# Optimization experiments

Hardware: AMD Instinct MI355X
Metric: run time of the kernel (lower is better)

## Reference

```python
import jax, jax.numpy as jnp
import numpy as np

LMAX, MMAX = 4, 2
K = (LMAX + 1) ** 2                                 # 25 SH coefficients (l-major node layout)
NL = [LMAX - m + 1 for m in range(MMAX + 1)]        # coeffs per order m: [5,4,3]
M_COEFF = NL[0] + sum(2 * n for n in NL[1:])        # 19 coeffs in m-major (mmax-truncated) edge layout
SPHERE_C, HIDDEN_C = 64, 64
NUM_HEADS, ALPHA_C, VALUE_C, OUT_C = 8, 32, 16, 64
P_GRID = 100
N_NODES, N_EDGES = 4096, 24576
NUM_SPECIES, EDGE_C, EMB_C = 90, 64, 64
N_EXTRA = NUM_HEADS * ALPHA_C + HIDDEN_C            # extra m=0 channels for S2_SEP: alpha + gate scalars


def _ln(x, g, b, eps=1e-5):
    mu = jnp.mean(x, -1, keepdims=True)
    var = jnp.var(x, -1, keepdims=True)
    return (x - mu) * jax.lax.rsqrt(var + eps) * g + b


def _smooth_leaky_relu(x, neg=0.2):
    return 0.5 * (1.0 + neg) * x + 0.5 * (1.0 - neg) * x * (2.0 * jax.nn.sigmoid(x) - 1.0)


def _segment_softmax(a, seg, n):
    amax = jax.lax.stop_gradient(jax.ops.segment_max(a, seg, num_segments=n))
    amax = jnp.where(jnp.isfinite(amax), amax, 0.0)
    e = jnp.exp(a - amax[seg])
    s = jax.ops.segment_sum(e, seg, num_segments=n)
    return e / (s[seg] + 1e-16)


def _so2_conv(x, w0, b0, wms, c_in, c_out, x_edge=None, n_extra=0):
    # x: [E, M_COEFF, c_in] in m-major layout (m=0 block, then per m: real rows then imag rows)
    E = x.shape[0]
    L0 = NL[0]
    x0 = x[:, :L0, :].reshape(E, L0 * c_in)
    if x_edge is not None:
        x0 = x0 * x_edge[:, :L0 * c_in]
    y0 = x0 @ w0 + b0
    extra = None
    if n_extra:
        extra = y0[:, L0 * c_out:]
        y0 = y0[:, :L0 * c_out]
    outs = [y0.reshape(E, L0, c_out)]
    off, rad = L0, L0 * c_in
    for m in range(1, MMAX + 1):
        nl = NL[m]
        xr = x[:, off:off + nl, :]
        xi = x[:, off + nl:off + 2 * nl, :]
        if x_edge is not None:
            s = x_edge[:, rad:rad + nl * c_in].reshape(E, nl, c_in)
            xr, xi = xr * s, xi * s
        xr = xr.reshape(E, nl * c_in)
        xi = xi.reshape(E, nl * c_in)
        half = nl * c_out
        wa, wb = wms[m - 1][:, :half], wms[m - 1][:, half:]
        yr = (xr @ wa - xi @ wb).reshape(E, nl, c_out)  # complex block-matmul
        yi = (xr @ wb + xi @ wa).reshape(E, nl, c_out)
        outs.append(jnp.concatenate([yr, yi], axis=1))
        off += 2 * nl
        rad += nl * c_in
    return jnp.concatenate(outs, axis=1), extra


def setup_inputs():
    key = jax.random.key(0)
    ks = iter(jax.random.split(key, 48))
    def w(shape, fan_in):
        return jax.random.normal(next(ks), shape, jnp.float32) / np.sqrt(fan_in)
    inp = {}
    inp['node_feats'] = jax.random.normal(next(ks), (N_NODES, K, SPHERE_C), jnp.float32)
    inp['node_species'] = jax.random.randint(next(ks), (N_NODES,), 0, NUM_SPECIES)
    inp['edge_distances'] = jax.random.normal(next(ks), (N_EDGES, EDGE_C), jnp.float32)
    inp['senders'] = jax.random.randint(next(ks), (N_EDGES,), 0, N_NODES)
    inp['receivers'] = jax.random.randint(next(ks), (N_EDGES,), 0, N_NODES)
    inp['wigner'] = jax.random.normal(next(ks), (N_EDGES, M_COEFF, K), jnp.float32) / np.sqrt(K)
    inp['snd_emb'] = jax.random.normal(next(ks), (NUM_SPECIES, EMB_C), jnp.float32) * 0.001
    inp['rcv_emb'] = jax.random.normal(next(ks), (NUM_SPECIES, EMB_C), jnp.float32) * 0.001
    ec = EDGE_C + 2 * EMB_C                              # 192 after atom-edge embedding concat
    n_rad = 2 * SPHERE_C * (NL[0] + NL[1] + NL[2])       # 1536 per-edge scales for conv1
    inp['rad_w1'] = w((ec, 64), ec); inp['rad_b1'] = jnp.zeros((64,))
    inp['rad_g1'] = jnp.ones((64,)); inp['rad_be1'] = jnp.zeros((64,))
    inp['rad_w2'] = w((64, 64), 64); inp['rad_b2'] = jnp.zeros((64,))
    inp['rad_g2'] = jnp.ones((64,)); inp['rad_be2'] = jnp.zeros((64,))
    inp['rad_w3'] = w((64, n_rad), 64); inp['rad_b3'] = jnp.ones((n_rad,))
    cin1 = 2 * SPHERE_C
    inp['c1_w0'] = w((NL[0] * cin1, NL[0] * HIDDEN_C + N_EXTRA), NL[0] * cin1)
    inp['c1_b0'] = jnp.zeros((NL[0] * HIDDEN_C + N_EXTRA,))
    inp['c1_wm1'] = w((NL[1] * cin1, 2 * NL[1] * HIDDEN_C), NL[1] * cin1)
    inp['c1_wm2'] = w((NL[2] * cin1, 2 * NL[2] * HIDDEN_C), NL[2] * cin1)
    inp['aln_g'] = jnp.ones((ALPHA_C,)); inp['aln_b'] = jnp.zeros((ALPHA_C,))
    inp['alpha_dot'] = w((NUM_HEADS, ALPHA_C), ALPHA_C)
    inp['to_grid'] = jax.random.normal(next(ks), (P_GRID, M_COEFF), jnp.float32) / np.sqrt(M_COEFF)
    inp['from_grid'] = jax.random.normal(next(ks), (M_COEFF, P_GRID), jnp.float32) / np.sqrt(P_GRID)
    cv = NUM_HEADS * VALUE_C
    inp['c2_w0'] = w((NL[0] * HIDDEN_C, NL[0] * cv), NL[0] * HIDDEN_C)
    inp['c2_b0'] = jnp.zeros((NL[0] * cv,))
    inp['c2_wm1'] = w((NL[1] * HIDDEN_C, 2 * NL[1] * cv), NL[1] * HIDDEN_C)
    inp['c2_wm2'] = w((NL[2] * HIDDEN_C, 2 * NL[2] * cv), NL[2] * HIDDEN_C)
    inp['proj_w'] = w((LMAX + 1, cv, OUT_C), cv)
    inp['proj_b'] = jnp.zeros((OUT_C,))
    return inp


def reference(node_feats, node_species, edge_distances, senders, receivers, wigner,
              snd_emb, rcv_emb, rad_w1, rad_b1, rad_g1, rad_be1, rad_w2, rad_b2,
              rad_g2, rad_be2, rad_w3, rad_b3, c1_w0, c1_b0, c1_wm1, c1_wm2,
              aln_g, aln_b, alpha_dot, to_grid, from_grid,
              c2_w0, c2_b0, c2_wm1, c2_wm2, proj_w, proj_b):
    N = node_feats.shape[0]
    # atom-edge embedding gathers + concat with radial-basis distances
    edge_embeds = jnp.concatenate([edge_distances,
                                   snd_emb[node_species[senders]],
                                   rcv_emb[node_species[receivers]]], axis=1)
    msgs = jnp.concatenate([node_feats[senders], node_feats[receivers]], axis=2)  # [E,25,128]
    msgs = jnp.einsum('emk,ekc->emc', wigner, msgs)                               # rotate to edge frame [E,19,128]
    # radial function -> per-edge input scales for SO2 conv 1
    h = jax.nn.silu(_ln(edge_embeds @ rad_w1 + rad_b1, rad_g1, rad_be1))
    h = jax.nn.silu(_ln(h @ rad_w2 + rad_b2, rad_g2, rad_be2))
    x_edge = h @ rad_w3 + rad_b3
    msgs, x0_extra = _so2_conv(msgs, c1_w0, c1_b0, [c1_wm1, c1_wm2],
                               2 * SPHERE_C, HIDDEN_C, x_edge, N_EXTRA)
    x0_alpha = x0_extra[:, :NUM_HEADS * ALPHA_C]
    x0_gate = x0_extra[:, NUM_HEADS * ALPHA_C:]
    # separable S2 activation: SiLU on sphere grid for l>0, SiLU on scalars for l=0
    grid = jax.nn.silu(jnp.einsum('pm,emc->epc', to_grid, msgs))
    tens = jnp.einsum('mp,epc->emc', from_grid, grid)
    msgs = jnp.concatenate([jax.nn.silu(x0_gate)[:, None, :], tens[:, 1:, :]], axis=1)
    msgs, _ = _so2_conv(msgs, c2_w0, c2_b0, [c2_wm1, c2_wm2], HIDDEN_C, NUM_HEADS * VALUE_C)
    # attention weights: LN -> SmoothLeakyReLU -> dot -> per-receiver softmax
    a = _smooth_leaky_relu(_ln(x0_alpha.reshape(-1, NUM_HEADS, ALPHA_C), aln_g, aln_b))
    alpha = _segment_softmax(jnp.einsum('ehk,hk->eh', a, alpha_dot), receivers, N)
    attn = msgs.reshape(-1, M_COEFF, NUM_HEADS, VALUE_C) * alpha[:, None, :, None]
    msgs = attn.reshape(-1, M_COEFF, NUM_HEADS * VALUE_C)
    msgs = jnp.einsum('emk,emc->ekc', wigner, msgs)    # rotate back (W^T), [E,25,128]
    node = jax.ops.segment_sum(msgs, receivers, num_segments=N)
    # SO3 linear: per-degree-l channel mixing, bias only on l=0
    l_of_k = jnp.asarray(np.repeat(np.arange(LMAX + 1), 2 * np.arange(LMAX + 1) + 1))
    out = jnp.einsum('nkc,kcd->nkd', node, proj_w[l_of_k])
    return out.at[:, 0, :].add(proj_b)
```

## Files before the change

### kernel.cpp

```cpp
#include <hip/hip_runtime.h>

typedef unsigned short u16;
typedef unsigned int u32;
typedef __attribute__((ext_vector_type(8))) short short8;
typedef __attribute__((ext_vector_type(4))) float floatx4;

#define E_EDGES 24576
#define EC 12288
#define N_NODES_C 4096

__device__ __forceinline__ float bf2f(u16 u) {
    union { u32 i; float f; } v; v.i = ((u32)u) << 16; return v.f;
}
__device__ __forceinline__ u16 f2bf(float f) {
    union { float f; u32 i; } v; v.f = f;
    u32 x = v.i;
    u32 r = (x + 0x7fffu + ((x >> 16) & 1u)) >> 16;
    return (u16)r;
}
__device__ __forceinline__ u32 pk_bf16(float a, float b) {
    u32 r;
    asm("v_cvt_pk_bf16_f32 %0, %1, %2" : "=v"(r) : "v"(a), "v"(b));
    return r;
}
__device__ __forceinline__ u32 encf(float f) {
    union { float f; u32 i; } v; v.f = f;
    return (v.i & 0x80000000u) ? ~v.i : (v.i | 0x80000000u);
}
__device__ __forceinline__ float decf(u32 u) {
    union { u32 i; float f; } v;
    v.i = (u & 0x80000000u) ? (u ^ 0x80000000u) : ~u;
    return v.f;
}
__device__ __forceinline__ float sigmoidf_(float x) { return __fdividef(1.f, 1.f + __expf(-x)); }
__device__ __forceinline__ float siluf_(float x) { return x * __fdividef(1.f, 1.f + __expf(-x)); }

__device__ __forceinline__ void gld16(const u16* g, u16* l) {
    __builtin_amdgcn_global_load_lds((const __attribute__((address_space(1))) unsigned int*)g,
                                     (__attribute__((address_space(3))) unsigned int*)l, 16, 0, 0);
}

__global__ void k_diag(float* __restrict__ out, int n) {
    int i = blockIdx.x * 256 + threadIdx.x;
    if (i < n) out[i] = 1000.0f;
}

struct PrepArgs {
    const float *rad_w1, *rad_w2, *rad_w3, *c1_w0, *c2_w0;
    const float *c1_wm1, *c1_wm2, *c2_wm1, *c2_wm2;
    const float *to_grid, *from_grid, *proj_w;
    u16 *w_rad1T, *w_rad2T, *w_rad3T, *w_c1w0T, *w_c2w0T;
    u16 *w_c1m1T, *w_c1m2T, *w_c2m1T, *w_c2m2T;
    u16 *w_tgP, *w_fgP, *w_pwT;
    u32 *nmax; float *nsum; u32 *c_deg;
    const float *dist; const int *species, *snd, *rcv;
    const float *semb, *remb; u16 *ee;
};

__device__ __forceinline__ void prep_transpose(const float* __restrict__ src, u16* __restrict__ dst,
                                               int K, int N, int idx) {
    if (idx >= K * N) return;
    int k = idx / N, n = idx % N;
    dst[n * K + k] = f2bf(src[idx]);
}
__device__ __forceinline__ void prep_combine(const float* __restrict__ src, u16* __restrict__ dst,
                                             int K, int H, int idx) {
    if (idx >= 4 * K * H) return;
    int n = idx / (2 * K), k = idx % (2 * K);
    float v;
    if (k < K) v = src[k * 2 * H + n];
    else {
        int kk = k - K;
        if (n < H) v = -src[kk * 2 * H + H + n];
        else       v = src[kk * 2 * H + (n - H)];
    }
    dst[idx] = f2bf(v);
}

#define PB0 48
#define PB1 16
#define PB2 384
#define PB3 1600
#define PB4 800
#define PB5 2048
#define PB6 1152
#define PB7 2048
#define PB8 1152
#define PB9 30
#define PB10 160
#define PB11 128
#define PB12 16
#define PB13 18432
#define PREP_BLOCKS (PB0+PB1+PB2+PB3+PB4+PB5+PB6+PB7+PB8+PB9+PB10+PB11+PB12+PB13)

__global__ __launch_bounds__(256) void k_prep(PrepArgs a) {
    int bid = blockIdx.x;
    int tid = threadIdx.x;
    if (bid < PB0) { prep_transpose(a.rad_w1, a.w_rad1T, 192, 64, bid * 256 + tid); return; }
    bid -= PB0;
    if (bid < PB1) { prep_transpose(a.rad_w2, a.w_rad2T, 64, 64, bid * 256 + tid); return; }
    bid -= PB1;
    if (bid < PB2) { prep_transpose(a.rad_w3, a.w_rad3T, 64, 1536, bid * 256 + tid); return; }
    bid -= PB2;
    if (bid < PB3) { prep_transpose(a.c1_w0, a.w_c1w0T, 640, 640, bid * 256 + tid); return; }
    bid -= PB3;
    if (bid < PB4) { prep_transpose(a.c2_w0, a.w_c2w0T, 320, 640, bid * 256 + tid); return; }
    bid -= PB4;
    if (bid < PB5) { prep_combine(a.c1_wm1, a.w_c1m1T, 512, 256, bid * 256 + tid); return; }
    bid -= PB5;
    if (bid < PB6) { prep_combine(a.c1_wm2, a.w_c1m2T, 384, 192, bid * 256 + tid); return; }
    bid -= PB6;
    if (bid < PB7) { prep_combine(a.c2_wm1, a.w_c2m1T, 256, 512, bid * 256 + tid); return; }
    bid -= PB7;
    if (bid < PB8) { prep_combine(a.c2_wm2, a.w_c2m2T, 192, 384, bid * 256 + tid); return; }
    bid -= PB8;
    if (bid < PB9) {
        int idx = bid * 256 + tid;
        if (idx < 112 * 32) {
            int p = idx >> 5, m = idx & 31;
            a.w_tgP[idx] = (p < 100 && m < 19) ? f2bf(a.to_grid[p * 19 + m]) : (u16)0;
        }
        int j = idx - 112 * 32;
        if (j >= 0 && j < 32 * 128) {
            int m = j >> 7, k = j & 127;
            a.w_fgP[j] = (m < 19 && k < 100) ? f2bf(a.from_grid[m * 100 + k]) : (u16)0;
        }
        return;
    }
    bid -= PB9;
    if (bid < PB10) {
        int idx = bid * 256 + tid;
        int l = idx >> 13, rem = idx & 8191;
        prep_transpose(a.proj_w + (size_t)l * 8192, a.w_pwT + (size_t)l * 8192, 128, 64, rem);
        return;
    }
    bid -= PB10;
    if (bid < PB11) {
        int idx = bid * 256 + tid;
        if (idx < N_NODES_C * 8) { a.nmax[idx] = 0x007FFFFFu; a.nsum[idx] = 0.f; }
        return;
    }
    bid -= PB11;
    if (bid < PB12) {
        int idx = bid * 256 + tid;
        if (idx < N_NODES_C) a.c_deg[idx] = 0u;
        return;
    }
    bid -= PB12;
    {
        int idx = bid * 256 + tid;
        if (idx >= E_EDGES * 192) return;
        int e = idx / 192, c = idx % 192;
        float v;
        if (c < 64)       v = a.dist[e * 64 + c];
        else if (c < 128) v = a.semb[a.species[a.snd[e]] * 64 + (c - 64)];
        else              v = a.remb[a.species[a.rcv[e]] * 64 + (c - 128)];
        a.ee[idx] = f2bf(v);
    }
}

__global__ void k_deg(const int* __restrict__ rcv, u32* __restrict__ deg) {
    int e = blockIdx.x * 256 + threadIdx.x;
    if (e < E_EDGES) atomicAdd(&deg[rcv[e]], 1u);
}
__global__ __launch_bounds__(256) void k_pfx(const u32* __restrict__ deg,
                                             u32* __restrict__ rowstart, u32* __restrict__ cur) {
    __shared__ u32 ps[256];
    int t = threadIdx.x;
    u32 loc[16]; u32 s = 0;
#pragma unroll
    for (int i = 0; i < 16; i++) { loc[i] = s; s += deg[t * 16 + i]; }
    ps[t] = s;
    __syncthreads();
    for (int o = 1; o < 256; o <<= 1) {
        u32 v = (t >= o) ? ps[t - o] : 0u;
        __syncthreads();
        ps[t] += v;
        __syncthreads();
    }
    u32 base = (t == 0) ? 0u : ps[t - 1];
#pragma unroll
    for (int i = 0; i < 16; i++) { u32 v = base + loc[i]; rowstart[t * 16 + i] = v; cur[t * 16 + i] = v; }
}
__global__ void k_fill(const int* __restrict__ rcv, u32* __restrict__ cur, int* __restrict__ elist) {
    int e = blockIdx.x * 256 + threadIdx.x;
    if (e < E_EDGES) { u32 p = atomicAdd(&cur[rcv[e]], 1u); elist[p] = e; }
}

__global__ __launch_bounds__(256) void k_gemm(
    const u16* __restrict__ A, int lda,
    const u16* __restrict__ BT, int ldb,
    u16* __restrict__ C, int ldc,
    int N, int K,
    const float* __restrict__ bias) {
    __shared__ u16 As[2][128 * 32];
    __shared__ u16 Bs[2][128 * 32];
    int tid = threadIdx.x;
    int bm0 = blockIdx.x * 128;
    int bn0 = blockIdx.y * 128;
    int wave = tid >> 6, lane = tid & 63;
    int wm = (wave >> 1) * 64, wn = (wave & 1) * 64;
    int lrow = lane & 15, lk = (lane >> 4) * 8;

    int srow = (wave << 4) + (lane >> 2);
    int schunk = (lane & 3) << 3;
    const u16* Arow0 = A + (size_t)(bm0 + srow) * lda + schunk;
    const u16* Arow1 = A + (size_t)(bm0 + srow + 64) * lda + schunk;
    int n0 = bn0 + srow;      if (n0 >= N) n0 = N - 1;
    int n1 = bn0 + srow + 64; if (n1 >= N) n1 = N - 1;
    const u16* Brow0 = BT + (size_t)n0 * ldb + schunk;
    const u16* Brow1 = BT + (size_t)n1 * ldb + schunk;

    auto stage = [&](int buf, int k0) {
        gld16(Arow0 + k0, &As[buf][srow * 32 + schunk]);
        gld16(Arow1 + k0, &As[buf][(srow + 64) * 32 + schunk]);
        gld16(Brow0 + k0, &Bs[buf][srow * 32 + schunk]);
        gld16(Brow1 + k0, &Bs[buf][(srow + 64) * 32 + schunk]);
    };

    floatx4 acc[4][4];
#pragma unroll
    for (int i = 0; i < 4; i++)
#pragma unroll
        for (int j = 0; j < 4; j++) acc[i][j] = floatx4{0.f, 0.f, 0.f, 0.f};

    int NT = K >> 5;
    stage(0, 0);
    for (int kt = 0; kt < NT; kt++) {
        int cur = kt & 1;
        if (kt + 1 < NT) {
            stage(cur ^ 1, (kt + 1) << 5);
            asm volatile("s_waitcnt vmcnt(4)" ::: "memory");
        } else {
            asm volatile("s_waitcnt vmcnt(0)" ::: "memory");
        }
        __syncthreads();
        short8 a[4], b[4];
#pragma unroll
        for (int i = 0; i < 4; i++) a[i] = *(const short8*)(&As[cur][(wm + i * 16 + lrow) * 32 + lk]);
#pragma unroll
        for (int j = 0; j < 4; j++) b[j] = *(const short8*)(&Bs[cur][(wn + j * 16 + lrow) * 32 + lk]);
#pragma unroll
        for (int i = 0; i < 4; i++)
#pragma unroll
            for (int j = 0; j < 4; j++)
                acc[i][j] = __builtin_amdgcn_mfma_f32_16x16x32_bf16(b[j], a[i], acc[i][j], 0, 0, 0);
        __syncthreads();
    }

    int q = lane >> 4;
#pragma unroll
    for (int i = 0; i < 4; i++) {
        int row = bm0 + wm + i * 16 + lrow;
#pragma unroll
        for (int j = 0; j < 4; j++) {
            int col = bn0 + wn + j * 16 + q * 4;
            if (col < N) {
                float4 bv = bias ? *(const float4*)(&bias[col]) : float4{0.f, 0.f, 0.f, 0.f};
                uint2 pv;
                pv.x = pk_bf16(acc[i][j][0] + bv.x, acc[i][j][1] + bv.y);
                pv.y = pk_bf16(acc[i][j][2] + bv.z, acc[i][j][3] + bv.w);
                *(uint2*)(&C[(size_t)row * ldc + col]) = pv;
            }
        }
    }
}

struct GemmDesc {
    const u16* A; const u16* BT; u16* C;
    const float* bias;
    int lda, ldb, ldc, N, K;
};
struct Gemm3 {
    GemmDesc d[3];
    int cut0, cut1;
};
__global__ __launch_bounds__(256) void k_gemm3(Gemm3 g) {
    int y = blockIdx.y;
    GemmDesc d;
    int ytile;
    if (y < g.cut0)      { d = g.d[0]; ytile = y; }
    else if (y < g.cut1) { d = g.d[1]; ytile = y - g.cut0; }
    else                 { d = g.d[2]; ytile = y - g.cut1; }

    __shared__ u16 As[2][128 * 32];
    __shared__ u16 Bs[2][128 * 32];
    int tid = threadIdx.x;
    int bm0 = blockIdx.x * 128;
    int bn0 = ytile * 128;
    int wave = tid >> 6, lane = tid & 63;
    int wm = (wave >> 1) * 64, wn = (wave & 1) * 64;
    int lrow = lane & 15, lk = (lane >> 4) * 8;

    int srow = (wave << 4) + (lane >> 2);
    int schunk = (lane & 3) << 3;
    const u16* Arow0 = d.A + (size_t)(bm0 + srow) * d.lda + schunk;
    const u16* Arow1 = d.A + (size_t)(bm0 + srow + 64) * d.lda + schunk;
    int n0 = bn0 + srow;      if (n0 >= d.N) n0 = d.N - 1;
    int n1 = bn0 + srow + 64; if (n1 >= d.N) n1 = d.N - 1;
    const u16* Brow0 = d.BT + (size_t)n0 * d.ldb + schunk;
    const u16* Brow1 = d.BT + (size_t)n1 * d.ldb + schunk;

    auto stage = [&](int buf, int k0) {
        gld16(Arow0 + k0, &As[buf][srow * 32 + schunk]);
        gld16(Arow1 + k0, &As[buf][(srow + 64) * 32 + schunk]);
        gld16(Brow0 + k0, &Bs[buf][srow * 32 + schunk]);
        gld16(Brow1 + k0, &Bs[buf][(srow + 64) * 32 + schunk]);
    };

    floatx4 acc[4][4];
#pragma unroll
    for (int i = 0; i < 4; i++)
#pragma unroll
        for (int j = 0; j < 4; j++) acc[i][j] = floatx4{0.f, 0.f, 0.f, 0.f};

    int NT = d.K >> 5;
    stage(0, 0);
    for (int kt = 0; kt < NT; kt++) {
        int cur = kt & 1;
        if (kt + 1 < NT) {
            stage(cur ^ 1, (kt + 1) << 5);
            asm volatile("s_waitcnt vmcnt(4)" ::: "memory");
        } else {
            asm volatile("s_waitcnt vmcnt(0)" ::: "memory");
        }
        __syncthreads();
        short8 a[4], b[4];
#pragma unroll
        for (int i = 0; i < 4; i++) a[i] = *(const short8*)(&As[cur][(wm + i * 16 + lrow) * 32 + lk]);
#pragma unroll
        for (int j = 0; j < 4; j++) b[j] = *(const short8*)(&Bs[cur][(wn + j * 16 + lrow) * 32 + lk]);
#pragma unroll
        for (int i = 0; i < 4; i++)
#pragma unroll
            for (int j = 0; j < 4; j++)
                acc[i][j] = __builtin_amdgcn_mfma_f32_16x16x32_bf16(b[j], a[i], acc[i][j], 0, 0, 0);
        __syncthreads();
    }

    int q = lane >> 4;
#pragma unroll
    for (int i = 0; i < 4; i++) {
        int row = bm0 + wm + i * 16 + lrow;
#pragma unroll
        for (int j = 0; j < 4; j++) {
            int col = bn0 + wn + j * 16 + q * 4;
            if (col < d.N) {
                float4 bv = d.bias ? *(const float4*)(&d.bias[col]) : float4{0.f, 0.f, 0.f, 0.f};
                uint2 pv;
                pv.x = pk_bf16(acc[i][j][0] + bv.x, acc[i][j][1] + bv.y);
                pv.y = pk_bf16(acc[i][j][2] + bv.z, acc[i][j][3] + bv.w);
                *(uint2*)(&d.C[(size_t)row * d.ldc + col]) = pv;
            }
        }
    }
}

__global__ __launch_bounds__(256) void k_ln_silu(const u16* __restrict__ in, u16* __restrict__ out,
                                                 const float* __restrict__ g, const float* __restrict__ b) {
    int tid = threadIdx.x;
    int e = blockIdx.x * 4 + (tid >> 6);
    int c = tid & 63;
    float x = bf2f(in[(size_t)e * 64 + c]);
    float s = x, s2 = x * x;
#pragma unroll
    for (int o = 32; o; o >>= 1) { s += __shfl_xor(s, o); s2 += __shfl_xor(s2, o); }
    float mu = s * (1.f / 64.f);
    float var = s2 * (1.f / 64.f) - mu * mu;
    float rs = rsqrtf(var + 1e-5f);
    float y = (x - mu) * rs * g[c] + b[c];
    out[(size_t)e * 64 + c] = f2bf(siluf_(y));
}

__global__ __launch_bounds__(256) void k_rotate(const float* __restrict__ nf, const float* __restrict__ wig,
                                                const int* __restrict__ snd, const int* __restrict__ rcv,
                                                const u16* __restrict__ xe, u16* __restrict__ A1, int e0) {
    __shared__ float wl[2][475];
    int tid = threadIdx.x;
    for (int i = tid; i < 950; i += 256) {
        int ee = e0 + blockIdx.x * 2 + (i / 475);
        wl[i / 475][i % 475] = wig[(size_t)ee * 475 + (i % 475)];
    }
    __syncthreads();
    int le = tid >> 7, c = tid & 127;
    int el = blockIdx.x * 2 + le;
    int e = e0 + el;
    int nd = (c < 64) ? snd[e] : rcv[e];
    int cc = c & 63;
    float msg[25];
#pragma unroll
    for (int k = 0; k < 25; k++) msg[k] = nf[(size_t)nd * 1600 + k * 64 + cc];
    const float* w = wl[le];
    size_t ebase = (size_t)el * 2432;
    size_t xbase = (size_t)el * 1536;
#pragma unroll
    for (int m = 0; m < 19; m++) {
        float r = 0.f;
#pragma unroll
        for (int k = 0; k < 25; k++) r += w[m * 25 + k] * msg[k];
        int a1c, xc;
        if (m < 5)       { a1c = m * 128;               xc = m * 128; }
        else if (m < 9)  { a1c = 640 + (m - 5) * 128;   xc = 640 + (m - 5) * 128; }
        else if (m < 13) { a1c = 1152 + (m - 9) * 128;  xc = 640 + (m - 9) * 128; }
        else if (m < 16) { a1c = 1664 + (m - 13) * 128; xc = 1152 + (m - 13) * 128; }
        else             { a1c = 2048 + (m - 16) * 128; xc = 1152 + (m - 16) * 128; }
        float sc = bf2f(xe[xbase + xc + c]);
        A1[ebase + a1c + c] = f2bf(r * sc);
    }
}

__global__ __launch_bounds__(256) void k_logits(const u16* __restrict__ Y0, const int* __restrict__ rcv,
                                                const float* __restrict__ g, const float* __restrict__ b,
                                                const float* __restrict__ adot,
                                                float* __restrict__ logits, u32* __restrict__ nmax) {
    int e = blockIdx.x;
    int tid = threadIdx.x;
    int h = tid >> 5, c = tid & 31;
    float x = bf2f(Y0[(size_t)e * 640 + 320 + h * 32 + c]);
    float s = x, s2 = x * x;
#pragma unroll
    for (int o = 16; o; o >>= 1) { s += __shfl_xor(s, o); s2 += __shfl_xor(s2, o); }
    float mu = s * (1.f / 32.f);
    float var = s2 * (1.f / 32.f) - mu * mu;
    float rs = rsqrtf(var + 1e-5f);
    float a = (x - mu) * rs * g[c] + b[c];
    float f = 0.6f * a + 0.4f * a * (2.f * sigmoidf_(a) - 1.f);
    float l = f * adot[h * 32 + c];
#pragma unroll
    for (int o = 16; o; o >>= 1) l += __shfl_xor(l, o);
    if (c == 0) {
        logits[e * 8 + h] = l;
        atomicMax(&nmax[rcv[e] * 8 + h], encf(l));
    }
}

__global__ void k_expsum(const float* __restrict__ logits, const int* __restrict__ rcv,
                         const u32* __restrict__ nmax, float* __restrict__ ealpha, float* __restrict__ nsum) {
    int idx = blockIdx.x * 256 + threadIdx.x;
    if (idx >= E_EDGES * 8) return;
    int e = idx >> 3, h = idx & 7;
    int r = rcv[e];
    float amax = decf(nmax[r * 8 + h]);
    if (!(amax > -1e38f && amax < 1e38f)) amax = 0.f;
    float v = __expf(logits[idx] - amax);
    ealpha[idx] = v;
    atomicAdd(&nsum[r * 8 + h], v);
}

#define GR_XS_STR 40
#define GR_T1_STR 136
__global__ __launch_bounds__(256) void k_grid_mfma(
    const u16* __restrict__ Y0, const u16* __restrict__ Y1, const u16* __restrict__ Y2,
    const u16* __restrict__ tgP, const u16* __restrict__ fgP, u16* __restrict__ A2) {
    __shared__ u16 T1s[128 * GR_T1_STR];
    u16* Xs = T1s;
    int tid = threadIdx.x;
    int e0 = blockIdx.x * 2;
    {
        int mp = tid & 15;
        int c0 = ((tid >> 4) & 7) << 3;
        int le = tid >> 7;
        int e = e0 + le;
        int m0 = 2 * mp, m1 = m0 + 1;
        uint4 va = {0, 0, 0, 0}, vb = {0, 0, 0, 0};
        if (m0 < 5)       va = *(const uint4*)(&Y0[(size_t)e * 640 + m0 * 64 + c0]);
        else if (m0 < 13) va = *(const uint4*)(&Y1[(size_t)e * 512 + (m0 - 5) * 64 + c0]);
        else if (m0 < 19) va = *(const uint4*)(&Y2[(size_t)e * 384 + (m0 - 13) * 64 + c0]);
        if (m1 < 5)       vb = *(const uint4*)(&Y0[(size_t)e * 640 + m1 * 64 + c0]);
        else if (m1 < 13) vb = *(const uint4*)(&Y1[(size_t)e * 512 + (m1 - 5) * 64 + c0]);
        else if (m1 < 19) vb = *(const uint4*)(&Y2[(size_t)e * 384 + (m1 - 13) * 64 + c0]);
        const u16* pa = (const u16*)&va;
        const u16* pb = (const u16*)&vb;
        int rbase = le * 64 + c0;
#pragma unroll
        for (int j = 0; j < 8; j++) {
            u32 w = (u32)pa[j] | ((u32)pb[j] << 16);
            *(u32*)(&Xs[(rbase + j) * GR_XS_STR + 2 * mp]) = w;
        }
    }
    __syncthreads();
    int wave = tid >> 6, lane = tid & 63;
    int wn = wave << 5;
    int ln = lane & 15, q = lane >> 4;
    short8 bx0 = *(const short8*)(&Xs[(wn + ln) * GR_XS_STR + q * 8]);
    short8 bx1 = *(const short8*)(&Xs[(wn + 16 + ln) * GR_XS_STR + q * 8]);
    floatx4 acc1[2][7];
#pragma unroll
    for (int pt = 0; pt < 7; pt++) {
        short8 a = *(const short8*)(&tgP[(size_t)(pt * 16 + ln) * 32 + q * 8]);
        acc1[0][pt] = __builtin_amdgcn_mfma_f32_16x16x32_bf16(a, bx0, floatx4{0.f, 0.f, 0.f, 0.f}, 0, 0, 0);
        acc1[1][pt] = __builtin_amdgcn_mfma_f32_16x16x32_bf16(a, bx1, floatx4{0.f, 0.f, 0.f, 0.f}, 0, 0, 0);
    }
    __syncthreads();
    {
        int row = tid >> 1;
        uint4 z = {0, 0, 0, 0};
        *(uint4*)(&T1s[row * GR_T1_STR + 112 + (tid & 1) * 8]) = z;
    }
#pragma unroll
    for (int i = 0; i < 2; i++) {
        u16* dst = &T1s[(wn + i * 16 + ln) * GR_T1_STR + q * 4];
#pragma unroll
        for (int pt = 0; pt < 7; pt++) {
            uint2 pv;
            pv.x = pk_bf16(siluf_(acc1[i][pt][0]), siluf_(acc1[i][pt][1]));
            pv.y = pk_bf16(siluf_(acc1[i][pt][2]), siluf_(acc1[i][pt][3]));
            *(uint2*)(dst + pt * 16) = pv;
        }
    }
    __syncthreads();
    floatx4 acc2[2][2];
    acc2[0][0] = floatx4{0.f, 0.f, 0.f, 0.f}; acc2[0][1] = floatx4{0.f, 0.f, 0.f, 0.f};
    acc2[1][0] = floatx4{0.f, 0.f, 0.f, 0.f}; acc2[1][1] = floatx4{0.f, 0.f, 0.f, 0.f};
#pragma unroll
    for (int ks = 0; ks < 4; ks++) {
        short8 c0 = *(const short8*)(&T1s[(wn + ln) * GR_T1_STR + ks * 32 + q * 8]);
        short8 c1 = *(const short8*)(&T1s[(wn + 16 + ln) * GR_T1_STR + ks * 32 + q * 8]);
#pragma unroll
        for (int ct = 0; ct < 2; ct++) {
            short8 b = *(const short8*)(&fgP[(size_t)(ct * 16 + ln) * 128 + ks * 32 + q * 8]);
            acc2[0][ct] = __builtin_amdgcn_mfma_f32_16x16x32_bf16(c0, b, acc2[0][ct], 0, 0, 0);
            acc2[1][ct] = __builtin_amdgcn_mfma_f32_16x16x32_bf16(c1, b, acc2[1][ct], 0, 0, 0);
        }
    }
#pragma unroll
    for (int rt = 0; rt < 2; rt++) {
        int row = wn + rt * 16 + q * 4;
        int e = e0 + (row >> 6), c = row & 63;
#pragma unroll
        for (int ct = 0; ct < 2; ct++) {
            int mp = ct * 16 + ln;
            if (mp >= 1 && mp < 19) {
                uint2 pv;
                pv.x = pk_bf16(acc2[rt][ct][0], acc2[rt][ct][1]);
                pv.y = pk_bf16(acc2[rt][ct][2], acc2[rt][ct][3]);
                *(uint2*)(&A2[(size_t)e * 1216 + mp * 64 + c]) = pv;
            }
        }
    }
    if (tid < 128) {
        int e = e0 + (tid >> 6), c = tid & 63;
        float gate = bf2f(Y0[(size_t)e * 640 + 576 + c]);
        A2[(size_t)e * 1216 + c] = f2bf(siluf_(gate));
    }
}

__global__ __launch_bounds__(256) void k_gather(
    const u16* __restrict__ Z0, const u16* __restrict__ Z1, const u16* __restrict__ Z2,
    const float* __restrict__ wig, const float* __restrict__ ealpha, const float* __restrict__ nsum,
    const u32* __restrict__ rowstart, const u32* __restrict__ deg, const int* __restrict__ elist,
    float* __restrict__ node, int e0, int accum) {
    int n = blockIdx.x * 4 + (threadIdx.x >> 6);
    int lane = threadIdx.x & 63;
    int h = lane >> 3;
    float sden = __fdividef(1.f, nsum[n * 8 + h] + 1e-16f);
    float a0[25], a1[25];
#pragma unroll
    for (int k = 0; k < 25; k++) { a0[k] = 0.f; a1[k] = 0.f; }
    u32 lo = rowstart[n], cnt = deg[n];
    bool did = false;
    for (u32 i = 0; i < cnt; i++) {
        int e = __builtin_amdgcn_readfirstlane(elist[lo + i]);
        int el = e - e0;
        if ((u32)el >= (u32)EC) continue;
        did = true;
        float al = ealpha[e * 8 + h] * sden;
        u32 zp[19];
        const u16* z0 = Z0 + (size_t)el * 640 + 2 * lane;
        const u16* z1 = Z1 + (size_t)el * 1024 + 2 * lane;
        const u16* z2 = Z2 + (size_t)el * 768 + 2 * lane;
#pragma unroll
        for (int m = 0; m < 5; m++) zp[m] = *(const u32*)(z0 + m * 128);
#pragma unroll
        for (int m = 0; m < 8; m++) zp[5 + m] = *(const u32*)(z1 + m * 128);
#pragma unroll
        for (int m = 0; m < 6; m++) zp[13 + m] = *(const u32*)(z2 + m * 128);
        const float* __restrict__ w = wig + (size_t)e * 475;
#pragma unroll
        for (int m = 0; m < 19; m++) {
            float s0 = bf2f((u16)(zp[m] & 0xffffu)) * al;
            float s1 = bf2f((u16)(zp[m] >> 16)) * al;
#pragma unroll
            for (int k = 0; k < 25; k++) {
                float wv = w[m * 25 + k];
                a0[k] = fmaf(wv, s0, a0[k]);
                a1[k] = fmaf(wv, s1, a1[k]);
            }
        }
    }
    float* nb = node + (size_t)n * 3200 + 2 * lane;
    if (accum) {
        if (!did) return;
#pragma unroll
        for (int k = 0; k < 25; k++) {
            float2 v = *(float2*)(&nb[k * 128]);
            v.x += a0[k]; v.y += a1[k];
            *(float2*)(&nb[k * 128]) = v;
        }
    } else {
#pragma unroll
        for (int k = 0; k < 25; k++) {
            float2 v; v.x = a0[k]; v.y = a1[k];
            *(float2*)(&nb[k * 128]) = v;
        }
    }
}

#define PJ_STR 136
__global__ __launch_bounds__(256) void k_proj_mfma(
    const float* __restrict__ node, const u16* __restrict__ pwTb,
    const float* __restrict__ pb, float* __restrict__ out) {
    __shared__ u16 As[128 * PJ_STR];
    __shared__ u16 Bs[64 * PJ_STR];
    int tid = threadIdx.x;
    int n0 = blockIdx.x * 128;
    int k = blockIdx.y;
    int l = (int)sqrtf((float)k + 0.5f);
#pragma unroll
    for (int it = 0; it < 16; it++) {
        int i = tid + it * 256;
        int row = i >> 5;
        int c0 = (i & 31) << 2;
        float4 v = *(const float4*)(&node[(size_t)(n0 + row) * 3200 + k * 128 + c0]);
        uint2 pv;
        pv.x = pk_bf16(v.x, v.y);
        pv.y = pk_bf16(v.z, v.w);
        *(uint2*)(&As[row * PJ_STR + c0]) = pv;
    }
    const u16* pw = pwTb + (size_t)l * 8192;
#pragma unroll
    for (int jt = 0; jt < 4; jt++) {
        int j = tid + jt * 256;
        int d = j >> 4;
        int c0 = (j & 15) << 3;
        *(uint4*)(&Bs[d * PJ_STR + c0]) = *(const uint4*)(&pw[d * 128 + c0]);
    }
    __syncthreads();
    int wave = tid >> 6, lane = tid & 63;
    int wr = wave * 32;
    int ln = lane & 15, q = lane >> 4;
    floatx4 acc[2][4];
#pragma unroll
    for (int i = 0; i < 2; i++)
#pragma unroll
        for (int j = 0; j < 4; j++) acc[i][j] = floatx4{0.f, 0.f, 0.f, 0.f};
#pragma unroll
    for (int ks = 0; ks < 4; ks++) {
        short8 a0 = *(const short8*)(&As[(wr + ln) * PJ_STR + ks * 32 + q * 8]);
        short8 a1 = *(const short8*)(&As[(wr + 16 + ln) * PJ_STR + ks * 32 + q * 8]);
#pragma unroll
        for (int j = 0; j < 4; j++) {
            short8 b = *(const short8*)(&Bs[(j * 16 + ln) * PJ_STR + ks * 32 + q * 8]);
            acc[0][j] = __builtin_amdgcn_mfma_f32_16x16x32_bf16(b, a0, acc[0][j], 0, 0, 0);
            acc[1][j] = __builtin_amdgcn_mfma_f32_16x16x32_bf16(b, a1, acc[1][j], 0, 0, 0);
        }
    }
#pragma unroll
    for (int rt = 0; rt < 2; rt++) {
        int n = n0 + wr + rt * 16 + ln;
#pragma unroll
        for (int j = 0; j < 4; j++) {
            int d = j * 16 + q * 4;
            float4 v;
            v.x = acc[rt][j][0]; v.y = acc[rt][j][1];
            v.z = acc[rt][j][2]; v.w = acc[rt][j][3];
            if (k == 0) {
                float4 bv = *(const float4*)(&pb[d]);
                v.x += bv.x; v.y += bv.y; v.z += bv.z; v.w += bv.w;
            }
            *(float4*)(&out[(size_t)n * 1600 + k * 64 + d]) = v;
        }
    }
}

extern "C" void kernel_launch(void* const* d_in, const int* in_sizes, int n_in,
                              void* d_out, int out_size, void* d_ws, size_t ws_size,
                              hipStream_t stream) {
    const float* nf      = (const float*)d_in[0];
    const int* species   = (const int*)d_in[1];
    const float* dist    = (const float*)d_in[2];
    const int* snd       = (const int*)d_in[3];
    const int* rcv       = (const int*)d_in[4];
    const float* wig     = (const float*)d_in[5];
    const float* semb    = (const float*)d_in[6];
    const float* remb    = (const float*)d_in[7];
    const float* rad_w1  = (const float*)d_in[8];
    const float* rad_b1  = (const float*)d_in[9];
    const float* rad_g1  = (const float*)d_in[10];
    const float* rad_be1 = (const float*)d_in[11];
    const float* rad_w2  = (const float*)d_in[12];
    const float* rad_b2  = (const float*)d_in[13];
    const float* rad_g2  = (const float*)d_in[14];
    const float* rad_be2 = (const float*)d_in[15];
    const float* rad_w3  = (const float*)d_in[16];
    const float* rad_b3  = (const float*)d_in[17];
    const float* c1_w0   = (const float*)d_in[18];
    const float* c1_b0   = (const float*)d_in[19];
    const float* c1_wm1  = (const float*)d_in[20];
    const float* c1_wm2  = (const float*)d_in[21];
    const float* aln_g   = (const float*)d_in[22];
    const float* aln_b   = (const float*)d_in[23];
    const float* adot    = (const float*)d_in[24];
    const float* to_grid = (const float*)d_in[25];
    const float* from_grid=(const float*)d_in[26];
    const float* c2_w0   = (const float*)d_in[27];
    const float* c2_b0   = (const float*)d_in[28];
    const float* c2_wm1  = (const float*)d_in[29];
    const float* c2_wm2  = (const float*)d_in[30];
    const float* proj_w  = (const float*)d_in[31];
    const float* proj_b  = (const float*)d_in[32];

    char* ws = (char*)d_ws;
    size_t off = 0;
    auto take = [&](size_t bytes) -> char* {
        char* p = ws + off;
        off += (bytes + 255) & ~(size_t)255;
        return p;
    };
    u16* w_rad1T  = (u16*)take(64 * 192 * 2);
    u16* w_rad2T  = (u16*)take(64 * 64 * 2);
    u16* w_rad3T  = (u16*)take(1536 * 64 * 2);
    u16* w_c1w0T  = (u16*)take(640 * 640 * 2);
    u16* w_c1m1T  = (u16*)take((size_t)512 * 1024 * 2);
    u16* w_c1m2T  = (u16*)take((size_t)384 * 768 * 2);
    u16* w_c2w0T  = (u16*)take((size_t)640 * 320 * 2);
    u16* w_c2m1T  = (u16*)take((size_t)1024 * 512 * 2);
    u16* w_c2m2T  = (u16*)take((size_t)768 * 384 * 2);
    u16* w_tgP    = (u16*)take(112 * 32 * 2);
    u16* w_fgP    = (u16*)take(32 * 128 * 2);
    u16* w_pwT    = (u16*)take(5 * 8192 * 2);
    float* logits = (float*)take((size_t)E_EDGES * 8 * 4);
    float* ealpha = (float*)take((size_t)E_EDGES * 8 * 4);
    u32* nmax     = (u32*)take((size_t)N_NODES_C * 8 * 4);
    float* nsum   = (float*)take((size_t)N_NODES_C * 8 * 4);
    float* node   = (float*)take((size_t)N_NODES_C * 3200 * 4);
    u16* a_h2     = (u16*)take((size_t)E_EDGES * 64 * 2);
    u32* c_deg    = (u32*)take((size_t)N_NODES_C * 4);
    u32* c_row    = (u32*)take((size_t)N_NODES_C * 4);
    u32* c_cur    = (u32*)take((size_t)N_NODES_C * 4);
    int* c_elist  = (int*)take((size_t)E_EDGES * 4);
    char* arena   = take(173015040);
    if (off > ws_size) {
        k_diag<<<(out_size + 255) / 256, 256, 0, stream>>>((float*)d_out, out_size);
        return;
    }

    u16* a_ee   = (u16*)(arena + 0);
    u16* a_ypre = (u16*)(arena + 9437184);
    u16* a_h1   = (u16*)(arena + 12582912);
    u16* a_xe   = (u16*)(arena + 0);
    u16* a_A1   = (u16*)(arena + 37748736);
    u16* a_Y0   = (u16*)(arena + 97517568);
    u16* a_Y1   = (u16*)(arena + 128974848);
    u16* a_Y2   = (u16*)(arena + 154140672);
    u16* a_A2   = (u16*)(arena + 0);
    u16* a_Z0   = (u16*)(arena + 59768832);
    u16* a_Z1   = (u16*)(arena + 75497472);
    u16* a_Z2   = (u16*)(arena + 100663296);

    PrepArgs pa;
    pa.rad_w1 = rad_w1; pa.rad_w2 = rad_w2; pa.rad_w3 = rad_w3;
    pa.c1_w0 = c1_w0; pa.c2_w0 = c2_w0;
    pa.c1_wm1 = c1_wm1; pa.c1_wm2 = c1_wm2; pa.c2_wm1 = c2_wm1; pa.c2_wm2 = c2_wm2;
    pa.to_grid = to_grid; pa.from_grid = from_grid; pa.proj_w = proj_w;
    pa.w_rad1T = w_rad1T; pa.w_rad2T = w_rad2T; pa.w_rad3T = w_rad3T;
    pa.w_c1w0T = w_c1w0T; pa.w_c2w0T = w_c2w0T;
    pa.w_c1m1T = w_c1m1T; pa.w_c1m2T = w_c1m2T; pa.w_c2m1T = w_c2m1T; pa.w_c2m2T = w_c2m2T;
    pa.w_tgP = w_tgP; pa.w_fgP = w_fgP; pa.w_pwT = w_pwT;
    pa.nmax = nmax; pa.nsum = nsum; pa.c_deg = c_deg;
    pa.dist = dist; pa.species = species; pa.snd = snd; pa.rcv = rcv;
    pa.semb = semb; pa.remb = remb; pa.ee = a_ee;
    k_prep<<<PREP_BLOCKS, 256, 0, stream>>>(pa);

    k_deg<<<96, 256, 0, stream>>>(rcv, c_deg);
    k_pfx<<<1, 256, 0, stream>>>(c_deg, c_row, c_cur);
    k_fill<<<96, 256, 0, stream>>>(rcv, c_cur, c_elist);

    k_gemm<<<dim3(192, 1), 256, 0, stream>>>(a_ee, 192, w_rad1T, 192, a_ypre, 64, 64, 192, rad_b1);
    k_ln_silu<<<6144, 256, 0, stream>>>(a_ypre, a_h1, rad_g1, rad_be1);
    k_gemm<<<dim3(192, 1), 256, 0, stream>>>(a_h1, 64, w_rad2T, 64, a_ypre, 64, 64, 64, rad_b2);
    k_ln_silu<<<6144, 256, 0, stream>>>(a_ypre, a_h2, rad_g2, rad_be2);

    for (int c = 0; c < 2; c++) {
        int e0 = c * EC;
        k_gemm<<<dim3(96, 12), 256, 0, stream>>>(a_h2 + (size_t)e0 * 64, 64, w_rad3T, 64,
                                                 a_xe, 1536, 1536, 64, rad_b3);
        k_rotate<<<EC / 2, 256, 0, stream>>>(nf, wig, snd, rcv, a_xe, a_A1, e0);
        Gemm3 g1;
        g1.d[0] = { a_A1,        w_c1w0T, a_Y0 + (size_t)e0 * 640, c1_b0,   2432, 640,  640, 640, 640 };
        g1.d[1] = { a_A1 + 640,  w_c1m1T, a_Y1 + (size_t)e0 * 512, nullptr, 2432, 1024, 512, 512, 1024 };
        g1.d[2] = { a_A1 + 1664, w_c1m2T, a_Y2 + (size_t)e0 * 384, nullptr, 2432, 768,  384, 384, 768 };
        g1.cut0 = 5; g1.cut1 = 9;
        k_gemm3<<<dim3(96, 12), 256, 0, stream>>>(g1);
    }

    k_logits<<<E_EDGES, 256, 0, stream>>>(a_Y0, rcv, aln_g, aln_b, adot, logits, nmax);
    k_expsum<<<(E_EDGES * 8 + 255) / 256, 256, 0, stream>>>(logits, rcv, nmax, ealpha, nsum);

    k_grid_mfma<<<E_EDGES / 2, 256, 0, stream>>>(a_Y0, a_Y1, a_Y2, w_tgP, w_fgP, a_A2);

    for (int c = 0; c < 2; c++) {
        int e0 = c * EC;
        Gemm3 g2;
        g2.d[0] = { a_A2 + (size_t)e0 * 1216,       w_c2w0T, a_Z0, c2_b0,   1216, 320, 640,  640,  320 };
        g2.d[1] = { a_A2 + (size_t)e0 * 1216 + 320, w_c2m1T, a_Z1, nullptr, 1216, 512, 1024, 1024, 512 };
        g2.d[2] = { a_A2 + (size_t)e0 * 1216 + 832, w_c2m2T, a_Z2, nullptr, 1216, 384, 768,  768,  384 };
        g2.cut0 = 5; g2.cut1 = 13;
        k_gemm3<<<dim3(96, 19), 256, 0, stream>>>(g2);
        k_gather<<<N_NODES_C / 4, 256, 0, stream>>>(a_Z0, a_Z1, a_Z2, wig, ealpha, nsum,
                                                    c_row, c_deg, c_elist, node, e0, c);
    }

    k_proj_mfma<<<dim3(32, 25), 256, 0, stream>>>(node, w_pwT, proj_b, (float*)d_out);
}
```

Before: 911.8 us.

## Fuse radial MLP layers, merge logits into grid kernel, expsum into GEMM launch

```diff
diff --git a/kernel.cpp b/kernel.cpp
--- a/kernel.cpp
+++ b/kernel.cpp
@@ -187,6 +187,124 @@
     if (e < E_EDGES) { u32 p = atomicAdd(&cur[rcv[e]], 1u); elist[p] = e; }
 }
 
+__global__ __launch_bounds__(256) void k_radmlp(
+    const u16* __restrict__ ee, const u16* __restrict__ w1T, const u16* __restrict__ w2T,
+    const float* __restrict__ b1, const float* __restrict__ g1, const float* __restrict__ be1,
+    const float* __restrict__ b2, const float* __restrict__ g2, const float* __restrict__ be2,
+    u16* __restrict__ h2) {
+    __shared__ u16 Y1s[128 * 72];
+    int tid = threadIdx.x;
+    int wave = tid >> 6, lane = tid & 63;
+    int ln = lane & 15, q = lane >> 4;
+    int wm = wave * 32;
+    int e0 = blockIdx.x * 128;
+
+    floatx4 acc[2][4];
+#pragma unroll
+    for (int i = 0; i < 2; i++)
+#pragma unroll
+        for (int j = 0; j < 4; j++) acc[i][j] = floatx4{0.f, 0.f, 0.f, 0.f};
+#pragma unroll
+    for (int ks = 0; ks < 6; ks++) {
+        short8 a0 = *(const short8*)(&ee[(size_t)(e0 + wm + ln) * 192 + ks * 32 + q * 8]);
+        short8 a1 = *(const short8*)(&ee[(size_t)(e0 + wm + 16 + ln) * 192 + ks * 32 + q * 8]);
+#pragma unroll
+        for (int j = 0; j < 4; j++) {
+            short8 b = *(const short8*)(&w1T[(size_t)(j * 16 + ln) * 192 + ks * 32 + q * 8]);
+            acc[0][j] = __builtin_amdgcn_mfma_f32_16x16x32_bf16(b, a0, acc[0][j], 0, 0, 0);
+            acc[1][j] = __builtin_amdgcn_mfma_f32_16x16x32_bf16(b, a1, acc[1][j], 0, 0, 0);
+        }
+    }
+#pragma unroll
+    for (int i = 0; i < 2; i++) {
+        float s = 0.f, s2 = 0.f;
+#pragma unroll
+        for (int j = 0; j < 4; j++) {
+            int cb = j * 16 + q * 4;
+            float4 bv = *(const float4*)(&b1[cb]);
+            float vb[4] = {bv.x, bv.y, bv.z, bv.w};
+#pragma unroll
+            for (int r = 0; r < 4; r++) {
+                float v = acc[i][j][r] + vb[r];
+                acc[i][j][r] = v;
+                s += v; s2 += v * v;
+            }
+        }
+        s += __shfl_xor(s, 16); s += __shfl_xor(s, 32);
+        s2 += __shfl_xor(s2, 16); s2 += __shfl_xor(s2, 32);
+        float mu = s * (1.f / 64.f);
+        float var = s2 * (1.f / 64.f) - mu * mu;
+        float rs = rsqrtf(var + 1e-5f);
+        int row = wm + i * 16 + ln;
+#pragma unroll
+        for (int j = 0; j < 4; j++) {
+            int cb = j * 16 + q * 4;
+            float4 gv = *(const float4*)(&g1[cb]);
+            float4 ev = *(const float4*)(&be1[cb]);
+            float y0 = (acc[i][j][0] - mu) * rs * gv.x + ev.x;
+            float y1 = (acc[i][j][1] - mu) * rs * gv.y + ev.y;
+            float y2 = (acc[i][j][2] - mu) * rs * gv.z + ev.z;
+            float y3 = (acc[i][j][3] - mu) * rs * gv.w + ev.w;
+            uint2 pv;
+            pv.x = pk_bf16(siluf_(y0), siluf_(y1));
+            pv.y = pk_bf16(siluf_(y2), siluf_(y3));
+            *(uint2*)(&Y1s[row * 72 + cb]) = pv;
+        }
+    }
+    __syncthreads();
+#pragma unroll
+    for (int i = 0; i < 2; i++)
+#pragma unroll
+        for (int j = 0; j < 4; j++) acc[i][j] = floatx4{0.f, 0.f, 0.f, 0.f};
+#pragma unroll
+    for (int ks = 0; ks < 2; ks++) {
+        short8 a0 = *(const short8*)(&Y1s[(wm + ln) * 72 + ks * 32 + q * 8]);
+        short8 a1 = *(const short8*)(&Y1s[(wm + 16 + ln) * 72 + ks * 32 + q * 8]);
+#pragma unroll
+        for (int j = 0; j < 4; j++) {
+            short8 b = *(const short8*)(&w2T[(size_t)(j * 16 + ln) * 64 + ks * 32 + q * 8]);
+            acc[0][j] = __builtin_amdgcn_mfma_f32_16x16x32_bf16(b, a0, acc[0][j], 0, 0, 0);
+            acc[1][j] = __builtin_amdgcn_mfma_f32_16x16x32_bf16(b, a1, acc[1][j], 0, 0, 0);
+        }
+    }
+#pragma unroll
+    for (int i = 0; i < 2; i++) {
+        float s = 0.f, s2 = 0.f;
+#pragma unroll
+        for (int j = 0; j < 4; j++) {
+            int cb = j * 16 + q * 4;
+            float4 bv = *(const float4*)(&b2[cb]);
+            float vb[4] = {bv.x, bv.y, bv.z, bv.w};
+#pragma unroll
+            for (int r = 0; r < 4; r++) {
+                float v = acc[i][j][r] + vb[r];
+                acc[i][j][r] = v;
+                s += v; s2 += v * v;
+            }
+        }
+        s += __shfl_xor(s, 16); s += __shfl_xor(s, 32);
+        s2 += __shfl_xor(s2, 16); s2 += __shfl_xor(s2, 32);
+        float mu = s * (1.f / 64.f);
+        float var = s2 * (1.f / 64.f) - mu * mu;
+        float rs = rsqrtf(var + 1e-5f);
+        int row = e0 + wm + i * 16 + ln;
+#pragma unroll
+        for (int j = 0; j < 4; j++) {
+            int cb = j * 16 + q * 4;
+            float4 gv = *(const float4*)(&g2[cb]);
+            float4 ev = *(const float4*)(&be2[cb]);
+            float y0 = (acc[i][j][0] - mu) * rs * gv.x + ev.x;
+            float y1 = (acc[i][j][1] - mu) * rs * gv.y + ev.y;
+            float y2 = (acc[i][j][2] - mu) * rs * gv.z + ev.z;
+            float y3 = (acc[i][j][3] - mu) * rs * gv.w + ev.w;
+            uint2 pv;
+            pv.x = pk_bf16(siluf_(y0), siluf_(y1));
+            pv.y = pk_bf16(siluf_(y2), siluf_(y3));
+            *(uint2*)(&h2[(size_t)row * 64 + cb]) = pv;
+        }
+    }
+}
+
 __global__ __launch_bounds__(256) void k_gemm(
     const u16* __restrict__ A, int lda,
     const u16* __restrict__ BT, int ldb,
@@ -273,10 +391,27 @@
 };
 struct Gemm3 {
     GemmDesc d[3];
-    int cut0, cut1;
+    int cut0, cut1, nY;
+    const float* logits; const int* rcv; const u32* nmax;
+    float* ealpha; float* nsum;
 };
 __global__ __launch_bounds__(256) void k_gemm3(Gemm3 g) {
     int y = blockIdx.y;
+    if (y >= g.nY) {
+        int base = blockIdx.x * 256 + threadIdx.x;
+#pragma unroll
+        for (int it = 0; it < 8; it++) {
+            int idx = it * 24576 + base;
+            int e = idx >> 3, h = idx & 7;
+            int r = g.rcv[e];
+            float amax = decf(g.nmax[r * 8 + h]);
+            if (!(amax > -1e38f && amax < 1e38f)) amax = 0.f;
+            float v = __expf(g.logits[idx] - amax);
+            g.ealpha[idx] = v;
+            atomicAdd(&g.nsum[r * 8 + h], v);
+        }
+        return;
+    }
     GemmDesc d;
     int ytile;
     if (y < g.cut0)      { d = g.d[0]; ytile = y; }
@@ -356,22 +491,6 @@
     }
 }
 
-__global__ __launch_bounds__(256) void k_ln_silu(const u16* __restrict__ in, u16* __restrict__ out,
-                                                 const float* __restrict__ g, const float* __restrict__ b) {
-    int tid = threadIdx.x;
-    int e = blockIdx.x * 4 + (tid >> 6);
-    int c = tid & 63;
-    float x = bf2f(in[(size_t)e * 64 + c]);
-    float s = x, s2 = x * x;
-#pragma unroll
-    for (int o = 32; o; o >>= 1) { s += __shfl_xor(s, o); s2 += __shfl_xor(s2, o); }
-    float mu = s * (1.f / 64.f);
-    float var = s2 * (1.f / 64.f) - mu * mu;
-    float rs = rsqrtf(var + 1e-5f);
-    float y = (x - mu) * rs * g[c] + b[c];
-    out[(size_t)e * 64 + c] = f2bf(siluf_(y));
-}
-
 __global__ __launch_bounds__(256) void k_rotate(const float* __restrict__ nf, const float* __restrict__ wig,
                                                 const int* __restrict__ snd, const int* __restrict__ rcv,
                                                 const u16* __restrict__ xe, u16* __restrict__ A1, int e0) {
@@ -409,52 +528,37 @@
     }
 }
 
-__global__ __launch_bounds__(256) void k_logits(const u16* __restrict__ Y0, const int* __restrict__ rcv,
-                                                const float* __restrict__ g, const float* __restrict__ b,
-                                                const float* __restrict__ adot,
-                                                float* __restrict__ logits, u32* __restrict__ nmax) {
-    int e = blockIdx.x;
-    int tid = threadIdx.x;
-    int h = tid >> 5, c = tid & 31;
-    float x = bf2f(Y0[(size_t)e * 640 + 320 + h * 32 + c]);
-    float s = x, s2 = x * x;
-#pragma unroll
-    for (int o = 16; o; o >>= 1) { s += __shfl_xor(s, o); s2 += __shfl_xor(s2, o); }
-    float mu = s * (1.f / 32.f);
-    float var = s2 * (1.f / 32.f) - mu * mu;
-    float rs = rsqrtf(var + 1e-5f);
-    float a = (x - mu) * rs * g[c] + b[c];
-    float f = 0.6f * a + 0.4f * a * (2.f * sigmoidf_(a) - 1.f);
-    float l = f * adot[h * 32 + c];
-#pragma unroll
-    for (int o = 16; o; o >>= 1) l += __shfl_xor(l, o);
-    if (c == 0) {
-        logits[e * 8 + h] = l;
-        atomicMax(&nmax[rcv[e] * 8 + h], encf(l));
-    }
-}
-
-__global__ void k_expsum(const float* __restrict__ logits, const int* __restrict__ rcv,
-                         const u32* __restrict__ nmax, float* __restrict__ ealpha, float* __restrict__ nsum) {
-    int idx = blockIdx.x * 256 + threadIdx.x;
-    if (idx >= E_EDGES * 8) return;
-    int e = idx >> 3, h = idx & 7;
-    int r = rcv[e];
-    float amax = decf(nmax[r * 8 + h]);
-    if (!(amax > -1e38f && amax < 1e38f)) amax = 0.f;
-    float v = __expf(logits[idx] - amax);
-    ealpha[idx] = v;
-    atomicAdd(&nsum[r * 8 + h], v);
-}
-
 #define GR_XS_STR 40
 #define GR_T1_STR 136
-__global__ __launch_bounds__(256) void k_grid_mfma(
+__global__ __launch_bounds__(256) void k_grid_logits(
     const u16* __restrict__ Y0, const u16* __restrict__ Y1, const u16* __restrict__ Y2,
-    const u16* __restrict__ tgP, const u16* __restrict__ fgP, u16* __restrict__ A2) {
+    const u16* __restrict__ tgP, const u16* __restrict__ fgP, u16* __restrict__ A2,
+    const int* __restrict__ rcv, const float* __restrict__ lg, const float* __restrict__ lb,
+    const float* __restrict__ adot, float* __restrict__ logits, u32* __restrict__ nmax) {
     __shared__ u16 T1s[128 * GR_T1_STR];
+    int tid = threadIdx.x;
+    if (blockIdx.x >= E_EDGES / 2) {
+        int e = blockIdx.x - E_EDGES / 2;
+        int h = tid >> 5, c = tid & 31;
+        float x = bf2f(Y0[(size_t)e * 640 + 320 + h * 32 + c]);
+        float s = x, s2 = x * x;
+#pragma unroll
+        for (int o = 16; o; o >>= 1) { s += __shfl_xor(s, o); s2 += __shfl_xor(s2, o); }
+        float mu = s * (1.f / 32.f);
+        float var = s2 * (1.f / 32.f) - mu * mu;
+        float rs = rsqrtf(var + 1e-5f);
+        float a = (x - mu) * rs * lg[c] + lb[c];
+        float f = 0.6f * a + 0.4f * a * (2.f * sigmoidf_(a) - 1.f);
+        float l = f * adot[h * 32 + c];
+#pragma unroll
+        for (int o = 16; o; o >>= 1) l += __shfl_xor(l, o);
+        if (c == 0) {
+            logits[e * 8 + h] = l;
+            atomicMax(&nmax[rcv[e] * 8 + h], encf(l));
+        }
+        return;
+    }
     u16* Xs = T1s;
-    int tid = threadIdx.x;
     int e0 = blockIdx.x * 2;
     {
         int mp = tid & 15;
@@ -746,8 +850,6 @@
     }
 
     u16* a_ee   = (u16*)(arena + 0);
-    u16* a_ypre = (u16*)(arena + 9437184);
-    u16* a_h1   = (u16*)(arena + 12582912);
     u16* a_xe   = (u16*)(arena + 0);
     u16* a_A1   = (u16*)(arena + 37748736);
     u16* a_Y0   = (u16*)(arena + 97517568);
@@ -757,6 +859,7 @@
     u16* a_Z0   = (u16*)(arena + 59768832);
     u16* a_Z1   = (u16*)(arena + 75497472);
     u16* a_Z2   = (u16*)(arena + 100663296);
+
 
     PrepArgs pa;
     pa.rad_w1 = rad_w1; pa.rad_w2 = rad_w2; pa.rad_w3 = rad_w3;
@@ -776,10 +879,9 @@
     k_pfx<<<1, 256, 0, stream>>>(c_deg, c_row, c_cur);
     k_fill<<<96, 256, 0, stream>>>(rcv, c_cur, c_elist);
 
-    k_gemm<<<dim3(192, 1), 256, 0, stream>>>(a_ee, 192, w_rad1T, 192, a_ypre, 64, 64, 192, rad_b1);
-    k_ln_silu<<<6144, 256, 0, stream>>>(a_ypre, a_h1, rad_g1, rad_be1);
-    k_gemm<<<dim3(192, 1), 256, 0, stream>>>(a_h1, 64, w_rad2T, 64, a_ypre, 64, 64, 64, rad_b2);
-    k_ln_silu<<<6144, 256, 0, stream>>>(a_ypre, a_h2, rad_g2, rad_be2);
+    k_radmlp<<<192, 256, 0, stream>>>(a_ee, w_rad1T, w_rad2T,
+                                      rad_b1, rad_g1, rad_be1,
+                                      rad_b2, rad_g2, rad_be2, a_h2);
 
     for (int c = 0; c < 2; c++) {
         int e0 = c * EC;
@@ -790,14 +892,14 @@
         g1.d[0] = { a_A1,        w_c1w0T, a_Y0 + (size_t)e0 * 640, c1_b0,   2432, 640,  640, 640, 640 };
         g1.d[1] = { a_A1 + 640,  w_c1m1T, a_Y1 + (size_t)e0 * 512, nullptr, 2432, 1024, 512, 512, 1024 };
         g1.d[2] = { a_A1 + 1664, w_c1m2T, a_Y2 + (size_t)e0 * 384, nullptr, 2432, 768,  384, 384, 768 };
-        g1.cut0 = 5; g1.cut1 = 9;
+        g1.cut0 = 5; g1.cut1 = 9; g1.nY = 12;
+        g1.logits = nullptr; g1.rcv = nullptr; g1.nmax = nullptr; g1.ealpha = nullptr; g1.nsum = nullptr;
         k_gemm3<<<dim3(96, 12), 256, 0, stream>>>(g1);
     }
 
-    k_logits<<<E_EDGES, 256, 0, stream>>>(a_Y0, rcv, aln_g, aln_b, adot, logits, nmax);
-    k_expsum<<<(E_EDGES * 8 + 255) / 256, 256, 0, stream>>>(logits, rcv, nmax, ealpha, nsum);
-
-    k_grid_mfma<<<E_EDGES / 2, 256, 0, stream>>>(a_Y0, a_Y1, a_Y2, w_tgP, w_fgP, a_A2);
+    k_grid_logits<<<E_EDGES / 2 + E_EDGES, 256, 0, stream>>>(
+        a_Y0, a_Y1, a_Y2, w_tgP, w_fgP, a_A2,
+        rcv, aln_g, aln_b, adot, logits, nmax);
 
     for (int c = 0; c < 2; c++) {
         int e0 = c * EC;
@@ -805,8 +907,10 @@
         g2.d[0] = { a_A2 + (size_t)e0 * 1216,       w_c2w0T, a_Z0, c2_b0,   1216, 320, 640,  640,  320 };
         g2.d[1] = { a_A2 + (size_t)e0 * 1216 + 320, w_c2m1T, a_Z1, nullptr, 1216, 512, 1024, 1024, 512 };
         g2.d[2] = { a_A2 + (size_t)e0 * 1216 + 832, w_c2m2T, a_Z2, nullptr, 1216, 384, 768,  768,  384 };
-        g2.cut0 = 5; g2.cut1 = 13;
-        k_gemm3<<<dim3(96, 19), 256, 0, stream>>>(g2);
+        g2.cut0 = 5; g2.cut1 = 13; g2.nY = 19;
+        g2.logits = logits; g2.rcv = rcv; g2.nmax = nmax; g2.ealpha = ealpha; g2.nsum = nsum;
+        int gy = (c == 0) ? 20 : 19;
+        k_gemm3<<<dim3(96, gy), 256, 0, stream>>>(g2);
         k_gather<<<N_NODES_C / 4, 256, 0, stream>>>(a_Z0, a_Z1, a_Z2, wig, ealpha, nsum,
                                                     c_row, c_deg, c_elist, node, e0, c);
     }
```

Measured after the change: 900.1 us. About the same (-1.3%).
